# Performance work log

Measured on AMD Instinct MI355X. Metric: run time of the kernel, lower is better.

## Reference

```python
import jax, jax.numpy as jnp
import numpy as np

TOP_K = 2


def setup_inputs() -> dict:
    key = jax.random.key(0)
    ks = jax.random.split(key, 5)
    T, H, I, E = 4096, 2048, 4096, 8
    scale = 0.02
    return {
        "hidden_states": jax.random.normal(ks[0], (T, H), dtype=jnp.float32),
        "router_logits": jax.random.normal(ks[1], (T, E), dtype=jnp.float32),
        "w1": jax.random.normal(ks[2], (E, I, H), dtype=jnp.float32) * scale,
        "w3": jax.random.normal(ks[3], (E, I, H), dtype=jnp.float32) * scale,
        "w2": jax.random.normal(ks[4], (E, H, I), dtype=jnp.float32) * scale,
    }


def reference(hidden_states, router_logits, w1, w3, w2):
    # hidden_states: [T, H], router_logits: [T, E]
    E = w1.shape[0]
    # Top-k routing with softmax renormalization over the selected logits.
    topk_vals, topk_idx = jax.lax.top_k(router_logits, TOP_K)  # [T, K]
    routing_weights = jax.nn.softmax(topk_vals, axis=-1)       # [T, K]
    # combine[t, e] = sum of routing weights of slots that picked expert e
    combine = jnp.sum(
        jnp.where(topk_idx[:, :, None] == jnp.arange(E)[None, None, :],
                  routing_weights[:, :, None], 0.0),
        axis=1)  # [T, E]
    out = jnp.zeros_like(hidden_states)
    for e in range(E):  # fixed small structural loop over experts
        gate = hidden_states @ w1[e].T        # [T, I]
        up = hidden_states @ w3[e].T          # [T, I]
        y = (jax.nn.silu(gate) * up) @ w2[e].T  # [T, H]
        out = out + combine[:, e, None] * y
    return out
```

## Files before the change

kernel.cpp:

```cpp
#include <hip/hip_runtime.h>
#include <stdint.h>

#define T_TOK 4096
#define H_DIM 2048
#define I_DIM 4096
#define N_EXP 8

typedef __attribute__((ext_vector_type(8))) short bf16x8;
typedef __attribute__((ext_vector_type(4))) float f32x4;
typedef __attribute__((ext_vector_type(8))) unsigned short u16x8;

__device__ __forceinline__ unsigned short f2bf(float x) {
    union { float f; unsigned u; } v; v.f = x;
    unsigned r = v.u + 0x7FFF + ((v.u >> 16) & 1);
    return (unsigned short)(r >> 16);
}

__device__ __forceinline__ void async_cp16(const void* g, const unsigned short* lds_base) {
    __builtin_amdgcn_global_load_lds(
        (const __attribute__((address_space(1))) unsigned*)g,
        (__attribute__((address_space(3))) unsigned*)(unsigned)(uintptr_t)lds_base,
        16, 0, 0);
}

__global__ void routing_kernel(const float* __restrict__ logits,
                               int* __restrict__ counts, int* __restrict__ offsets,
                               int* __restrict__ btok, float* __restrict__ bw,
                               int* __restrict__ tok2slot) {
    __shared__ int s_cnt[N_EXP];
    __shared__ int s_off[N_EXP];
    __shared__ int s_cur[N_EXP];
    const int tid = threadIdx.x;
    if (tid < N_EXP) s_cnt[tid] = 0;
    __syncthreads();

    int e0a[16], e1a[16]; float w0a[16], w1a[16];
    #pragma unroll
    for (int it = 0; it < 16; ++it) {
        int t = tid + it * 256;
        float l[8];
        #pragma unroll
        for (int e = 0; e < 8; ++e) l[e] = logits[t * 8 + e];
        int b0 = 0; float v0 = l[0];
        #pragma unroll
        for (int e = 1; e < 8; ++e) if (l[e] > v0) { v0 = l[e]; b0 = e; }
        int b1 = (b0 == 0) ? 1 : 0; float v1 = l[b1];
        #pragma unroll
        for (int e = 0; e < 8; ++e) if (e != b0 && l[e] > v1) { v1 = l[e]; b1 = e; }
        float w0 = 1.0f / (1.0f + __expf(v1 - v0));
        e0a[it] = b0; e1a[it] = b1; w0a[it] = w0; w1a[it] = 1.0f - w0;
        atomicAdd(&s_cnt[b0], 1);
        atomicAdd(&s_cnt[b1], 1);
    }
    __syncthreads();
    if (tid == 0) {
        int acc = 0;
        for (int e = 0; e < N_EXP; ++e) { s_off[e] = acc; s_cur[e] = acc; acc += s_cnt[e]; }
    }
    __syncthreads();
    if (tid < N_EXP) { counts[tid] = s_cnt[tid]; offsets[tid] = s_off[tid]; }
    #pragma unroll
    for (int it = 0; it < 16; ++it) {
        int t = tid + it * 256;
        int p0 = atomicAdd(&s_cur[e0a[it]], 1);
        btok[p0] = t; bw[p0] = w0a[it];
        int p1 = atomicAdd(&s_cur[e1a[it]], 1);
        btok[p1] = t; bw[p1] = w1a[it];
        tok2slot[2 * t] = p0;
        tok2slot[2 * t + 1] = p1;
    }
}

__global__ void cvt_kernel(const float* __restrict__ x, unsigned short* __restrict__ xb) {
    int i = blockIdx.x * blockDim.x + threadIdx.x;
    float4 v = ((const float4*)x)[i];
    ushort4 o;
    o.x = f2bf(v.x); o.y = f2bf(v.y); o.z = f2bf(v.z); o.w = f2bf(v.w);
    ((ushort4*)xb)[i] = o;
}


__global__ __launch_bounds__(256, 2)
void gemm1f_kernel(const unsigned short* __restrict__ Xb,
                   const unsigned short* __restrict__ W1b,
                   const unsigned short* __restrict__ W3b,
                   const int* __restrict__ counts,
                   const int* __restrict__ offsets,
                   const int* __restrict__ btok,
                   unsigned short* __restrict__ hbuf) {
    const int e = blockIdx.z;
    const int ne = counts[e];
    const int mt = blockIdx.y;
    if (mt * 128 >= ne) return;
    const int nt = blockIdx.x;
    const int off = offsets[e];

    __shared__ unsigned short sA[128 * 32];
    __shared__ unsigned short sB1[128 * 32];
    __shared__ unsigned short sB3[128 * 32];
    __shared__ int s_tok[128];

    const int tid = threadIdx.x;
    if (tid < 128) {
        int slot = mt * 128 + tid;
        s_tok[tid] = btok[off + ((slot < ne) ? slot : 0)];
    }
    __syncthreads();

    const int lane = tid & 63;
    const int wv = tid >> 6;
    const int wm = (wv >> 1) << 6;
    const int wn = (wv & 1) << 6;
    const int q = lane >> 4;
    const int c = lane & 15;

    const int srow = wv * 32 + (lane >> 2);
    const int cc = (lane & 3) * 8;

    const unsigned short* gA0 = Xb + (size_t)s_tok[srow] * H_DIM + cc;
    const unsigned short* gA1 = Xb + (size_t)s_tok[srow + 16] * H_DIM + cc;
    const size_t wrow = (size_t)e * I_DIM + nt * 128 + srow;
    const unsigned short* gW1a = W1b + wrow * H_DIM + cc;
    const unsigned short* gW1b_ = W1b + (wrow + 16) * H_DIM + cc;
    const unsigned short* gW3a = W3b + wrow * H_DIM + cc;
    const unsigned short* gW3b_ = W3b + (wrow + 16) * H_DIM + cc;

    const unsigned short* dA0 = &sA[1024 * wv];
    const unsigned short* dA1 = &sA[1024 * wv + 512];
    const unsigned short* dB1a = &sB1[1024 * wv];
    const unsigned short* dB1b = &sB1[1024 * wv + 512];
    const unsigned short* dB3a = &sB3[1024 * wv];
    const unsigned short* dB3b = &sB3[1024 * wv + 512];

    f32x4 accg[4][4], accu[4][4];
    const f32x4 zero = {0.0f, 0.0f, 0.0f, 0.0f};
    #pragma unroll
    for (int i = 0; i < 4; ++i)
        #pragma unroll
        for (int j = 0; j < 4; ++j) { accg[i][j] = zero; accu[i][j] = zero; }

    for (int kt = 0; kt < H_DIM; kt += 32) {
        __syncthreads();
        async_cp16(gA0 + kt, dA0);
        async_cp16(gA1 + kt, dA1);
        async_cp16(gW1a + kt, dB1a);
        async_cp16(gW1b_ + kt, dB1b);
        async_cp16(gW3a + kt, dB3a);
        async_cp16(gW3b_ + kt, dB3b);
        __syncthreads();

        bf16x8 af[4], b1f[4], b3f[4];
        #pragma unroll
        for (int i = 0; i < 4; ++i)
            af[i] = *(const bf16x8*)(&sA[(wm + i * 16 + c) * 32 + q * 8]);
        #pragma unroll
        for (int j = 0; j < 4; ++j) {
            b1f[j] = *(const bf16x8*)(&sB1[(wn + j * 16 + c) * 32 + q * 8]);
            b3f[j] = *(const bf16x8*)(&sB3[(wn + j * 16 + c) * 32 + q * 8]);
        }
        #pragma unroll
        for (int i = 0; i < 4; ++i)
            #pragma unroll
            for (int j = 0; j < 4; ++j) {
                accg[i][j] = __builtin_amdgcn_mfma_f32_16x16x32_bf16(af[i], b1f[j], accg[i][j], 0, 0, 0);
                accu[i][j] = __builtin_amdgcn_mfma_f32_16x16x32_bf16(af[i], b3f[j], accu[i][j], 0, 0, 0);
            }
    }

    #pragma unroll
    for (int i = 0; i < 4; ++i) {
        #pragma unroll
        for (int r = 0; r < 4; ++r) {
            int mloc = wm + i * 16 + q * 4 + r;
            int slot = mt * 128 + mloc;
            if (slot < ne) {
                size_t rowbase = (size_t)(off + slot) * I_DIM + nt * 128 + wn;
                #pragma unroll
                for (int j = 0; j < 4; ++j) {
                    float g = accg[i][j][r];
                    float u = accu[i][j][r];
                    float val = (g / (1.0f + __expf(-g))) * u;
                    hbuf[rowbase + j * 16 + c] = f2bf(val);
                }
            }
        }
    }
}

__global__ __launch_bounds__(256, 2)
void gemm2f_kernel(const unsigned short* __restrict__ hbuf,
                   const unsigned short* __restrict__ W2b,
                   const int* __restrict__ counts,
                   const int* __restrict__ offsets,
                   float* __restrict__ ybuf) {
    const int e = blockIdx.z;
    const int ne = counts[e];
    const int mt = blockIdx.y;
    if (mt * 128 >= ne) return;
    const int nt = blockIdx.x;
    const int off = offsets[e];

    __shared__ unsigned short sA[128 * 32];
    __shared__ unsigned short sB[128 * 32];

    const int tid = threadIdx.x;
    const int lane = tid & 63;
    const int wv = tid >> 6;
    const int wm = (wv >> 1) << 6;
    const int wn = (wv & 1) << 6;
    const int q = lane >> 4;
    const int c = lane & 15;

    const int srow = wv * 32 + (lane >> 2);
    const int cc = (lane & 3) * 8;

    int slotA0 = mt * 128 + srow;      if (slotA0 >= ne) slotA0 = ne - 1;
    int slotA1 = mt * 128 + srow + 16; if (slotA1 >= ne) slotA1 = ne - 1;
    const unsigned short* gA0 = hbuf + (size_t)(off + slotA0) * I_DIM + cc;
    const unsigned short* gA1 = hbuf + (size_t)(off + slotA1) * I_DIM + cc;
    const size_t wrow = (size_t)e * H_DIM + nt * 128 + srow;
    const unsigned short* gB0 = W2b + wrow * I_DIM + cc;
    const unsigned short* gB1 = W2b + (wrow + 16) * I_DIM + cc;

    const unsigned short* dA0 = &sA[1024 * wv];
    const unsigned short* dA1 = &sA[1024 * wv + 512];
    const unsigned short* dB0 = &sB[1024 * wv];
    const unsigned short* dB1 = &sB[1024 * wv + 512];

    f32x4 acc[4][4];
    const f32x4 zero = {0.0f, 0.0f, 0.0f, 0.0f};
    #pragma unroll
    for (int i = 0; i < 4; ++i)
        #pragma unroll
        for (int j = 0; j < 4; ++j) acc[i][j] = zero;

    for (int kt = 0; kt < I_DIM; kt += 32) {
        __syncthreads();
        async_cp16(gA0 + kt, dA0);
        async_cp16(gA1 + kt, dA1);
        async_cp16(gB0 + kt, dB0);
        async_cp16(gB1 + kt, dB1);
        __syncthreads();

        bf16x8 af[4], bfr[4];
        #pragma unroll
        for (int i = 0; i < 4; ++i)
            af[i] = *(const bf16x8*)(&sA[(wm + i * 16 + c) * 32 + q * 8]);
        #pragma unroll
        for (int j = 0; j < 4; ++j)
            bfr[j] = *(const bf16x8*)(&sB[(wn + j * 16 + c) * 32 + q * 8]);
        #pragma unroll
        for (int i = 0; i < 4; ++i)
            #pragma unroll
            for (int j = 0; j < 4; ++j)
                acc[i][j] = __builtin_amdgcn_mfma_f32_16x16x32_bf16(af[i], bfr[j], acc[i][j], 0, 0, 0);
    }

    #pragma unroll
    for (int i = 0; i < 4; ++i) {
        #pragma unroll
        for (int r = 0; r < 4; ++r) {
            int mloc = wm + i * 16 + q * 4 + r;
            int slot = mt * 128 + mloc;
            if (slot < ne) {
                float* obase = ybuf + (size_t)(off + slot) * H_DIM + nt * 128 + wn;
                #pragma unroll
                for (int j = 0; j < 4; ++j)
                    obase[j * 16 + c] = acc[i][j][r];
            }
        }
    }
}

__global__ void combine_kernel(const float* __restrict__ ybuf,
                               const float* __restrict__ bw,
                               const int* __restrict__ tok2slot,
                               float* __restrict__ out) {
    int i = blockIdx.x * blockDim.x + threadIdx.x;
    int t = i >> 9;
    int h4 = i & 511;
    int p0 = tok2slot[2 * t], p1 = tok2slot[2 * t + 1];
    float w0 = bw[p0], w1 = bw[p1];
    float4 a = ((const float4*)(ybuf + (size_t)p0 * H_DIM))[h4];
    float4 b = ((const float4*)(ybuf + (size_t)p1 * H_DIM))[h4];
    float4 o;
    o.x = w0 * a.x + w1 * b.x;
    o.y = w0 * a.y + w1 * b.y;
    o.z = w0 * a.z + w1 * b.z;
    o.w = w0 * a.w + w1 * b.w;
    ((float4*)(out + (size_t)t * H_DIM))[h4] = o;
}


__global__ __launch_bounds__(256, 2)
void gemm1_kernel(const unsigned short* __restrict__ Xb,
                  const float* __restrict__ W1,
                  const float* __restrict__ W3,
                  const int* __restrict__ counts,
                  const int* __restrict__ offsets,
                  const int* __restrict__ btok,
                  unsigned short* __restrict__ hbuf) {
    const int e = blockIdx.z;
    const int ne = counts[e];
    const int mt = blockIdx.y;
    if (mt * 128 >= ne) return;
    const int nt = blockIdx.x;
    const int off = offsets[e];

    __shared__ unsigned short sA[128][32];
    __shared__ unsigned short sB1[128][32];
    __shared__ unsigned short sB3[128][32];
    __shared__ int s_tok[128];

    const int tid = threadIdx.x;
    if (tid < 128) {
        int slot = mt * 128 + tid;
        s_tok[tid] = (slot < ne) ? btok[off + slot] : -1;
    }

    const float* __restrict__ pB1 = W1 + (size_t)e * I_DIM * H_DIM + (size_t)(nt * 128) * H_DIM;
    const float* __restrict__ pB3 = W3 + (size_t)e * I_DIM * H_DIM + (size_t)(nt * 128) * H_DIM;

    const int lane = tid & 63;
    const int wv = tid >> 6;
    const int wm = (wv >> 1) << 6;
    const int wn = (wv & 1) << 6;
    const int q = lane >> 4;
    const int c = lane & 15;

    f32x4 accg[4][4], accu[4][4];
    const f32x4 zero = {0.0f, 0.0f, 0.0f, 0.0f};
    #pragma unroll
    for (int i = 0; i < 4; ++i)
        #pragma unroll
        for (int j = 0; j < 4; ++j) { accg[i][j] = zero; accu[i][j] = zero; }

    const int srow = tid >> 2;
    const int schunk = (tid & 3) * 8;

    for (int kt = 0; kt < H_DIM; kt += 32) {
        __syncthreads();
        #pragma unroll
        for (int p = 0; p < 2; ++p) {
            int r = srow + p * 64;
            int tok = s_tok[r];
            u16x8 av = {0, 0, 0, 0, 0, 0, 0, 0};
            if (tok >= 0)
                av = *(const u16x8*)(Xb + (size_t)tok * H_DIM + kt + schunk);
            *(u16x8*)(&sA[r][schunk]) = av;

            const float* b1 = pB1 + (size_t)r * H_DIM + kt + schunk;
            float4 x0 = *(const float4*)(b1);
            float4 x1 = *(const float4*)(b1 + 4);
            u16x8 bv;
            bv[0] = f2bf(x0.x); bv[1] = f2bf(x0.y); bv[2] = f2bf(x0.z); bv[3] = f2bf(x0.w);
            bv[4] = f2bf(x1.x); bv[5] = f2bf(x1.y); bv[6] = f2bf(x1.z); bv[7] = f2bf(x1.w);
            *(u16x8*)(&sB1[r][schunk]) = bv;

            const float* b3 = pB3 + (size_t)r * H_DIM + kt + schunk;
            float4 y0 = *(const float4*)(b3);
            float4 y1 = *(const float4*)(b3 + 4);
            u16x8 cv;
            cv[0] = f2bf(y0.x); cv[1] = f2bf(y0.y); cv[2] = f2bf(y0.z); cv[3] = f2bf(y0.w);
            cv[4] = f2bf(y1.x); cv[5] = f2bf(y1.y); cv[6] = f2bf(y1.z); cv[7] = f2bf(y1.w);
            *(u16x8*)(&sB3[r][schunk]) = cv;
        }
        __syncthreads();

        bf16x8 af[4], b1f[4], b3f[4];
        #pragma unroll
        for (int i = 0; i < 4; ++i)
            af[i] = *(const bf16x8*)(&sA[wm + i * 16 + c][q * 8]);
        #pragma unroll
        for (int j = 0; j < 4; ++j) {
            b1f[j] = *(const bf16x8*)(&sB1[wn + j * 16 + c][q * 8]);
            b3f[j] = *(const bf16x8*)(&sB3[wn + j * 16 + c][q * 8]);
        }
        #pragma unroll
        for (int i = 0; i < 4; ++i)
            #pragma unroll
            for (int j = 0; j < 4; ++j) {
                accg[i][j] = __builtin_amdgcn_mfma_f32_16x16x32_bf16(af[i], b1f[j], accg[i][j], 0, 0, 0);
                accu[i][j] = __builtin_amdgcn_mfma_f32_16x16x32_bf16(af[i], b3f[j], accu[i][j], 0, 0, 0);
            }
    }

    #pragma unroll
    for (int i = 0; i < 4; ++i) {
        #pragma unroll
        for (int r = 0; r < 4; ++r) {
            int mloc = wm + i * 16 + q * 4 + r;
            int slot = mt * 128 + mloc;
            if (slot < ne) {
                size_t rowbase = (size_t)(off + slot) * I_DIM + nt * 128 + wn;
                #pragma unroll
                for (int j = 0; j < 4; ++j) {
                    float g = accg[i][j][r];
                    float u = accu[i][j][r];
                    float val = (g / (1.0f + __expf(-g))) * u;
                    hbuf[rowbase + j * 16 + c] = f2bf(val);
                }
            }
        }
    }
}

__global__ __launch_bounds__(256, 2)
void gemm2_kernel(const unsigned short* __restrict__ hbuf,
                  const float* __restrict__ W2,
                  const int* __restrict__ counts,
                  const int* __restrict__ offsets,
                  const int* __restrict__ btok,
                  const float* __restrict__ bw,
                  float* __restrict__ out) {
    const int e = blockIdx.z;
    const int ne = counts[e];
    const int mt = blockIdx.y;
    if (mt * 128 >= ne) return;
    const int nt = blockIdx.x;
    const int off = offsets[e];

    __shared__ unsigned short sA[128][32];
    __shared__ unsigned short sB[128][32];

    const int tid = threadIdx.x;
    const int lane = tid & 63;
    const int wv = tid >> 6;
    const int wm = (wv >> 1) << 6;
    const int wn = (wv & 1) << 6;
    const int q = lane >> 4;
    const int c = lane & 15;

    const float* __restrict__ pB = W2 + (size_t)e * H_DIM * I_DIM + (size_t)(nt * 128) * I_DIM;

    f32x4 acc[4][4];
    const f32x4 zero = {0.0f, 0.0f, 0.0f, 0.0f};
    #pragma unroll
    for (int i = 0; i < 4; ++i)
        #pragma unroll
        for (int j = 0; j < 4; ++j) acc[i][j] = zero;

    const int srow = tid >> 2;
    const int schunk = (tid & 3) * 8;

    for (int kt = 0; kt < I_DIM; kt += 32) {
        __syncthreads();
        #pragma unroll
        for (int p = 0; p < 2; ++p) {
            int r = srow + p * 64;
            int slot = mt * 128 + r;
            u16x8 av = {0, 0, 0, 0, 0, 0, 0, 0};
            if (slot < ne)
                av = *(const u16x8*)(hbuf + (size_t)(off + slot) * I_DIM + kt + schunk);
            *(u16x8*)(&sA[r][schunk]) = av;

            const float* b = pB + (size_t)r * I_DIM + kt + schunk;
            float4 x0 = *(const float4*)(b);
            float4 x1 = *(const float4*)(b + 4);
            u16x8 bv;
            bv[0] = f2bf(x0.x); bv[1] = f2bf(x0.y); bv[2] = f2bf(x0.z); bv[3] = f2bf(x0.w);
            bv[4] = f2bf(x1.x); bv[5] = f2bf(x1.y); bv[6] = f2bf(x1.z); bv[7] = f2bf(x1.w);
            *(u16x8*)(&sB[r][schunk]) = bv;
        }
        __syncthreads();

        bf16x8 af[4], bfr[4];
        #pragma unroll
        for (int i = 0; i < 4; ++i)
            af[i] = *(const bf16x8*)(&sA[wm + i * 16 + c][q * 8]);
        #pragma unroll
        for (int j = 0; j < 4; ++j)
            bfr[j] = *(const bf16x8*)(&sB[wn + j * 16 + c][q * 8]);
        #pragma unroll
        for (int i = 0; i < 4; ++i)
            #pragma unroll
            for (int j = 0; j < 4; ++j)
                acc[i][j] = __builtin_amdgcn_mfma_f32_16x16x32_bf16(af[i], bfr[j], acc[i][j], 0, 0, 0);
    }

    #pragma unroll
    for (int i = 0; i < 4; ++i) {
        #pragma unroll
        for (int r = 0; r < 4; ++r) {
            int mloc = wm + i * 16 + q * 4 + r;
            int slot = mt * 128 + mloc;
            if (slot < ne) {
                int tok = btok[off + slot];
                float wgt = bw[off + slot];
                float* obase = out + (size_t)tok * H_DIM + nt * 128 + wn;
                #pragma unroll
                for (int j = 0; j < 4; ++j)
                    atomicAdd(obase + j * 16 + c, wgt * acc[i][j][r]);
            }
        }
    }
}


extern "C" void kernel_launch(void* const* d_in, const int* in_sizes, int n_in,
                              void* d_out, int out_size, void* d_ws, size_t ws_size,
                              hipStream_t stream) {
    const float* hs = (const float*)d_in[0];
    const float* rl = (const float*)d_in[1];
    const float* w1 = (const float*)d_in[2];
    const float* w3 = (const float*)d_in[3];
    const float* w2 = (const float*)d_in[4];
    float* out = (float*)d_out;

    char* ws = (char*)d_ws;
    int*   counts   = (int*)(ws);
    int*   offsets  = (int*)(ws + 256);
    int*   btok     = (int*)(ws + 4096);
    float* bw       = (float*)(ws + 36864);
    int*   tok2slot = (int*)(ws + 69632);

    const size_t MB = 1ull << 20;
    const size_t NEED_A = 529 * MB;

    if (ws_size >= NEED_A) {
        unsigned short* Xb   = (unsigned short*)(ws + 1 * MB);
        unsigned short* hbuf = (unsigned short*)(ws + 17 * MB);
        float*          ybuf = (float*)(ws + 81 * MB);
        unsigned short* w1b  = (unsigned short*)(ws + 145 * MB);
        unsigned short* w3b  = (unsigned short*)(ws + 273 * MB);
        unsigned short* w2b  = (unsigned short*)(ws + 401 * MB);

        routing_kernel<<<1, 256, 0, stream>>>(rl, counts, offsets, btok, bw, tok2slot);

        cvt_kernel<<<(T_TOK * H_DIM / 4) / 256, 256, 0, stream>>>(hs, Xb);
        int wn4 = N_EXP * I_DIM * H_DIM / 4;
        cvt_kernel<<<wn4 / 256, 256, 0, stream>>>(w1, w1b);
        cvt_kernel<<<wn4 / 256, 256, 0, stream>>>(w3, w3b);
        cvt_kernel<<<wn4 / 256, 256, 0, stream>>>(w2, w2b);

        gemm1f_kernel<<<dim3(I_DIM / 128, 64, N_EXP), 256, 0, stream>>>(
            Xb, w1b, w3b, counts, offsets, btok, hbuf);

        gemm2f_kernel<<<dim3(H_DIM / 128, 64, N_EXP), 256, 0, stream>>>(
            hbuf, w2b, counts, offsets, ybuf);

        combine_kernel<<<(T_TOK * (H_DIM / 4)) / 256, 256, 0, stream>>>(
            ybuf, bw, tok2slot, out);
    } else {
        unsigned short* Xb   = (unsigned short*)(ws + 1 * MB);
        unsigned short* hbuf = (unsigned short*)(ws + 32 * MB);

        hipMemsetAsync(out, 0, (size_t)T_TOK * H_DIM * sizeof(float), stream);

        routing_kernel<<<1, 256, 0, stream>>>(rl, counts, offsets, btok, bw, tok2slot);

        cvt_kernel<<<(T_TOK * H_DIM / 4) / 256, 256, 0, stream>>>(hs, Xb);

        gemm1_kernel<<<dim3(I_DIM / 128, T_TOK / 128, N_EXP), 256, 0, stream>>>(
            Xb, w1, w3, counts, offsets, btok, hbuf);

        gemm2_kernel<<<dim3(H_DIM / 128, T_TOK / 128, N_EXP), 256, 0, stream>>>(
            hbuf, w2, counts, offsets, btok, bw, out);
    }
}
```

Baseline: 1.369 ms.

## Triple-buffer MoE GEMMs with larger 256-row tiles, LDS swizzle, and interleaved prefetch

```diff
diff --git a/kernel.cpp b/kernel.cpp
--- a/kernel.cpp
+++ b/kernel.cpp
@@ -80,8 +80,8 @@
 }
 
 
-__global__ __launch_bounds__(256, 2)
-void gemm1f_kernel(const unsigned short* __restrict__ Xb,
+__global__ __launch_bounds__(512, 2)
+void gemm1p_kernel(const unsigned short* __restrict__ Xb,
                    const unsigned short* __restrict__ W1b,
                    const unsigned short* __restrict__ W3b,
                    const int* __restrict__ counts,
@@ -91,19 +91,19 @@
     const int e = blockIdx.z;
     const int ne = counts[e];
     const int mt = blockIdx.y;
-    if (mt * 128 >= ne) return;
+    if (mt * 256 >= ne) return;
     const int nt = blockIdx.x;
     const int off = offsets[e];
 
-    __shared__ unsigned short sA[128 * 32];
-    __shared__ unsigned short sB1[128 * 32];
-    __shared__ unsigned short sB3[128 * 32];
-    __shared__ int s_tok[128];
+    __shared__ unsigned short sA[3][256 * 32];
+    __shared__ unsigned short sB1[3][128 * 32];
+    __shared__ unsigned short sB3[3][128 * 32];
+    __shared__ int s_tok[256];
 
     const int tid = threadIdx.x;
-    if (tid < 128) {
-        int slot = mt * 128 + tid;
-        s_tok[tid] = btok[off + ((slot < ne) ? slot : 0)];
+    if (tid < 256) {
+        int slot = mt * 256 + tid;
+        s_tok[tid] = btok[off + ((slot < ne) ? slot : (ne - 1))];
     }
     __syncthreads();
 
@@ -113,24 +113,23 @@
     const int wn = (wv & 1) << 6;
     const int q = lane >> 4;
     const int c = lane & 15;
-
-    const int srow = wv * 32 + (lane >> 2);
-    const int cc = (lane & 3) * 8;
-
-    const unsigned short* gA0 = Xb + (size_t)s_tok[srow] * H_DIM + cc;
-    const unsigned short* gA1 = Xb + (size_t)s_tok[srow + 16] * H_DIM + cc;
+    const int xq = q ^ ((c >> 1) & 3);
+
+    const int aoff = (wm + c) * 32 + xq * 8;
+    const int boff = (wn + c) * 32 + xq * 8;
+
+    const int srow = wv * 16 + (lane >> 2);
+    const int sg = (lane & 3) ^ ((lane >> 3) & 3);
+
+    const unsigned short* gA0 = Xb + (size_t)s_tok[srow] * H_DIM + sg * 8;
+    const unsigned short* gA1 = Xb + (size_t)s_tok[srow + 128] * H_DIM + sg * 8;
     const size_t wrow = (size_t)e * I_DIM + nt * 128 + srow;
-    const unsigned short* gW1a = W1b + wrow * H_DIM + cc;
-    const unsigned short* gW1b_ = W1b + (wrow + 16) * H_DIM + cc;
-    const unsigned short* gW3a = W3b + wrow * H_DIM + cc;
-    const unsigned short* gW3b_ = W3b + (wrow + 16) * H_DIM + cc;
-
-    const unsigned short* dA0 = &sA[1024 * wv];
-    const unsigned short* dA1 = &sA[1024 * wv + 512];
-    const unsigned short* dB1a = &sB1[1024 * wv];
-    const unsigned short* dB1b = &sB1[1024 * wv + 512];
-    const unsigned short* dB3a = &sB3[1024 * wv];
-    const unsigned short* dB3b = &sB3[1024 * wv + 512];
+    const unsigned short* gB1 = W1b + wrow * H_DIM + sg * 8;
+    const unsigned short* gB3 = W3b + wrow * H_DIM + sg * 8;
+
+    const int dofsA0 = wv * 512;
+    const int dofsA1 = 4096 + wv * 512;
+    const int dofsB  = wv * 512;
 
     f32x4 accg[4][4], accu[4][4];
     const f32x4 zero = {0.0f, 0.0f, 0.0f, 0.0f};
@@ -139,32 +138,66 @@
         #pragma unroll
         for (int j = 0; j < 4; ++j) { accg[i][j] = zero; accu[i][j] = zero; }
 
-    for (int kt = 0; kt < H_DIM; kt += 32) {
-        __syncthreads();
-        async_cp16(gA0 + kt, dA0);
-        async_cp16(gA1 + kt, dA1);
-        async_cp16(gW1a + kt, dB1a);
-        async_cp16(gW1b_ + kt, dB1b);
-        async_cp16(gW3a + kt, dB3a);
-        async_cp16(gW3b_ + kt, dB3b);
-        __syncthreads();
-
-        bf16x8 af[4], b1f[4], b3f[4];
-        #pragma unroll
-        for (int i = 0; i < 4; ++i)
-            af[i] = *(const bf16x8*)(&sA[(wm + i * 16 + c) * 32 + q * 8]);
-        #pragma unroll
-        for (int j = 0; j < 4; ++j) {
-            b1f[j] = *(const bf16x8*)(&sB1[(wn + j * 16 + c) * 32 + q * 8]);
-            b3f[j] = *(const bf16x8*)(&sB3[(wn + j * 16 + c) * 32 + q * 8]);
-        }
+    async_cp16(gA0,      &sA[0][dofsA0]);
+    async_cp16(gB1,      &sB1[0][dofsB]);
+    async_cp16(gA1,      &sA[0][dofsA1]);
+    async_cp16(gB3,      &sB3[0][dofsB]);
+    async_cp16(gA0 + 32, &sA[1][dofsA0]);
+    async_cp16(gB1 + 32, &sB1[1][dofsB]);
+    async_cp16(gA1 + 32, &sA[1][dofsA1]);
+    async_cp16(gB3 + 32, &sB3[1][dofsB]);
+    asm volatile("s_waitcnt vmcnt(4)" ::: "memory");
+    __builtin_amdgcn_s_barrier();
+    __builtin_amdgcn_sched_barrier(0);
+
+    const int NT = H_DIM / 32;
+    for (int t = 0; t < NT; ++t) {
+        const int cur = t % 3;
+        const int nx2 = (t + 2) % 3;
+        const bool stg = (t + 2) < NT;
+        const int kt2 = (t + 2) * 32;
+
+        bf16x8 af[4], b1f[4];
+        #pragma unroll
+        for (int i = 0; i < 4; ++i) af[i] = *(const bf16x8*)(&sA[cur][aoff + i * 512]);
+        #pragma unroll
+        for (int j = 0; j < 4; ++j) b1f[j] = *(const bf16x8*)(&sB1[cur][boff + j * 512]);
+        if (stg) {
+            async_cp16(gA0 + kt2, &sA[nx2][dofsA0]);
+            async_cp16(gB1 + kt2, &sB1[nx2][dofsB]);
+        }
+        __builtin_amdgcn_s_barrier();
+        __builtin_amdgcn_s_setprio(1);
         #pragma unroll
         for (int i = 0; i < 4; ++i)
             #pragma unroll
-            for (int j = 0; j < 4; ++j) {
+            for (int j = 0; j < 4; ++j)
                 accg[i][j] = __builtin_amdgcn_mfma_f32_16x16x32_bf16(af[i], b1f[j], accg[i][j], 0, 0, 0);
+        __builtin_amdgcn_s_setprio(0);
+        __builtin_amdgcn_s_barrier();
+
+        bf16x8 b3f[4];
+        #pragma unroll
+        for (int j = 0; j < 4; ++j) b3f[j] = *(const bf16x8*)(&sB3[cur][boff + j * 512]);
+        if (stg) {
+            async_cp16(gA1 + kt2, &sA[nx2][dofsA1]);
+            async_cp16(gB3 + kt2, &sB3[nx2][dofsB]);
+        }
+        __builtin_amdgcn_s_barrier();
+        __builtin_amdgcn_s_setprio(1);
+        #pragma unroll
+        for (int i = 0; i < 4; ++i)
+            #pragma unroll
+            for (int j = 0; j < 4; ++j)
                 accu[i][j] = __builtin_amdgcn_mfma_f32_16x16x32_bf16(af[i], b3f[j], accu[i][j], 0, 0, 0);
-            }
+        __builtin_amdgcn_s_setprio(0);
+
+        if (t + 1 < NT) {
+            if (stg) asm volatile("s_waitcnt vmcnt(4)" ::: "memory");
+            else     asm volatile("s_waitcnt vmcnt(0)" ::: "memory");
+            __builtin_amdgcn_s_barrier();
+            __builtin_amdgcn_sched_barrier(0);
+        }
     }
 
     #pragma unroll
@@ -172,7 +205,7 @@
         #pragma unroll
         for (int r = 0; r < 4; ++r) {
             int mloc = wm + i * 16 + q * 4 + r;
-            int slot = mt * 128 + mloc;
+            int slot = mt * 256 + mloc;
             if (slot < ne) {
                 size_t rowbase = (size_t)(off + slot) * I_DIM + nt * 128 + wn;
                 #pragma unroll
@@ -187,8 +220,8 @@
     }
 }
 
-__global__ __launch_bounds__(256, 2)
-void gemm2f_kernel(const unsigned short* __restrict__ hbuf,
+__global__ __launch_bounds__(512, 2)
+void gemm2p_kernel(const unsigned short* __restrict__ hbuf,
                    const unsigned short* __restrict__ W2b,
                    const int* __restrict__ counts,
                    const int* __restrict__ offsets,
@@ -196,74 +229,116 @@
     const int e = blockIdx.z;
     const int ne = counts[e];
     const int mt = blockIdx.y;
-    if (mt * 128 >= ne) return;
+    if (mt * 256 >= ne) return;
     const int nt = blockIdx.x;
     const int off = offsets[e];
 
-    __shared__ unsigned short sA[128 * 32];
-    __shared__ unsigned short sB[128 * 32];
+    __shared__ unsigned short sA[3][256 * 32];
+    __shared__ unsigned short sB[3][256 * 32];
 
     const int tid = threadIdx.x;
     const int lane = tid & 63;
     const int wv = tid >> 6;
-    const int wm = (wv >> 1) << 6;
-    const int wn = (wv & 1) << 6;
+    const int wm = (wv >> 2) << 7;
+    const int wn = (wv & 3) << 6;
     const int q = lane >> 4;
     const int c = lane & 15;
-
-    const int srow = wv * 32 + (lane >> 2);
-    const int cc = (lane & 3) * 8;
-
-    int slotA0 = mt * 128 + srow;      if (slotA0 >= ne) slotA0 = ne - 1;
-    int slotA1 = mt * 128 + srow + 16; if (slotA1 >= ne) slotA1 = ne - 1;
-    const unsigned short* gA0 = hbuf + (size_t)(off + slotA0) * I_DIM + cc;
-    const unsigned short* gA1 = hbuf + (size_t)(off + slotA1) * I_DIM + cc;
-    const size_t wrow = (size_t)e * H_DIM + nt * 128 + srow;
-    const unsigned short* gB0 = W2b + wrow * I_DIM + cc;
-    const unsigned short* gB1 = W2b + (wrow + 16) * I_DIM + cc;
-
-    const unsigned short* dA0 = &sA[1024 * wv];
-    const unsigned short* dA1 = &sA[1024 * wv + 512];
-    const unsigned short* dB0 = &sB[1024 * wv];
-    const unsigned short* dB1 = &sB[1024 * wv + 512];
-
-    f32x4 acc[4][4];
+    const int xq = q ^ ((c >> 1) & 3);
+
+    const int aoff = (wm + c) * 32 + xq * 8;
+    const int boff = (wn + c) * 32 + xq * 8;
+
+    const int srow = wv * 16 + (lane >> 2);
+    const int sg = (lane & 3) ^ ((lane >> 3) & 3);
+
+    int slot0 = mt * 256 + srow;        if (slot0 >= ne) slot0 = ne - 1;
+    int slot1 = mt * 256 + srow + 128;  if (slot1 >= ne) slot1 = ne - 1;
+    const unsigned short* gA0 = hbuf + (size_t)(off + slot0) * I_DIM + sg * 8;
+    const unsigned short* gA1 = hbuf + (size_t)(off + slot1) * I_DIM + sg * 8;
+    const size_t wrow = (size_t)e * H_DIM + nt * 256 + srow;
+    const unsigned short* gB0 = W2b + wrow * I_DIM + sg * 8;
+    const unsigned short* gB1 = W2b + (wrow + 128) * I_DIM + sg * 8;
+
+    const int dofs0 = wv * 512;
+    const int dofs1 = 4096 + wv * 512;
+
+    f32x4 acc[8][4];
     const f32x4 zero = {0.0f, 0.0f, 0.0f, 0.0f};
     #pragma unroll
-    for (int i = 0; i < 4; ++i)
+    for (int i = 0; i < 8; ++i)
         #pragma unroll
         for (int j = 0; j < 4; ++j) acc[i][j] = zero;
 
-    for (int kt = 0; kt < I_DIM; kt += 32) {
-        __syncthreads();
-        async_cp16(gA0 + kt, dA0);
-        async_cp16(gA1 + kt, dA1);
-        async_cp16(gB0 + kt, dB0);
-        async_cp16(gB1 + kt, dB1);
-        __syncthreads();
+    async_cp16(gA0,      &sA[0][dofs0]);
+    async_cp16(gB0,      &sB[0][dofs0]);
+    async_cp16(gA1,      &sA[0][dofs1]);
+    async_cp16(gB1,      &sB[0][dofs1]);
+    async_cp16(gA0 + 32, &sA[1][dofs0]);
+    async_cp16(gB0 + 32, &sB[1][dofs0]);
+    async_cp16(gA1 + 32, &sA[1][dofs1]);
+    async_cp16(gB1 + 32, &sB[1][dofs1]);
+    asm volatile("s_waitcnt vmcnt(4)" ::: "memory");
+    __builtin_amdgcn_s_barrier();
+    __builtin_amdgcn_sched_barrier(0);
+
+    const int NT = I_DIM / 32;
+    for (int t = 0; t < NT; ++t) {
+        const int cur = t % 3;
+        const int nx2 = (t + 2) % 3;
+        const bool stg = (t + 2) < NT;
+        const int kt2 = (t + 2) * 32;
 
         bf16x8 af[4], bfr[4];
         #pragma unroll
-        for (int i = 0; i < 4; ++i)
-            af[i] = *(const bf16x8*)(&sA[(wm + i * 16 + c) * 32 + q * 8]);
-        #pragma unroll
-        for (int j = 0; j < 4; ++j)
-            bfr[j] = *(const bf16x8*)(&sB[(wn + j * 16 + c) * 32 + q * 8]);
+        for (int i = 0; i < 4; ++i) af[i] = *(const bf16x8*)(&sA[cur][aoff + i * 512]);
+        #pragma unroll
+        for (int j = 0; j < 4; ++j) bfr[j] = *(const bf16x8*)(&sB[cur][boff + j * 512]);
+        if (stg) {
+            async_cp16(gA0 + kt2, &sA[nx2][dofs0]);
+            async_cp16(gB0 + kt2, &sB[nx2][dofs0]);
+        }
+        __builtin_amdgcn_s_barrier();
+        __builtin_amdgcn_s_setprio(1);
         #pragma unroll
         for (int i = 0; i < 4; ++i)
             #pragma unroll
             for (int j = 0; j < 4; ++j)
                 acc[i][j] = __builtin_amdgcn_mfma_f32_16x16x32_bf16(af[i], bfr[j], acc[i][j], 0, 0, 0);
-    }
-
-    #pragma unroll
-    for (int i = 0; i < 4; ++i) {
+        __builtin_amdgcn_s_setprio(0);
+        __builtin_amdgcn_s_barrier();
+
+        bf16x8 af2[4];
+        #pragma unroll
+        for (int i = 0; i < 4; ++i) af2[i] = *(const bf16x8*)(&sA[cur][aoff + (i + 4) * 512]);
+        if (stg) {
+            async_cp16(gA1 + kt2, &sA[nx2][dofs1]);
+            async_cp16(gB1 + kt2, &sB[nx2][dofs1]);
+        }
+        __builtin_amdgcn_s_barrier();
+        __builtin_amdgcn_s_setprio(1);
+        #pragma unroll
+        for (int i = 0; i < 4; ++i)
+            #pragma unroll
+            for (int j = 0; j < 4; ++j)
+                acc[i + 4][j] = __builtin_amdgcn_mfma_f32_16x16x32_bf16(af2[i], bfr[j], acc[i + 4][j], 0, 0, 0);
+        __builtin_amdgcn_s_setprio(0);
+
+        if (t + 1 < NT) {
+            if (stg) asm volatile("s_waitcnt vmcnt(4)" ::: "memory");
+            else     asm volatile("s_waitcnt vmcnt(0)" ::: "memory");
+            __builtin_amdgcn_s_barrier();
+            __builtin_amdgcn_sched_barrier(0);
+        }
+    }
+
+    #pragma unroll
+    for (int i = 0; i < 8; ++i) {
         #pragma unroll
         for (int r = 0; r < 4; ++r) {
             int mloc = wm + i * 16 + q * 4 + r;
-            int slot = mt * 128 + mloc;
+            int slot = mt * 256 + mloc;
             if (slot < ne) {
-                float* obase = ybuf + (size_t)(off + slot) * H_DIM + nt * 128 + wn;
+                float* obase = ybuf + (size_t)(off + slot) * H_DIM + nt * 256 + wn;
                 #pragma unroll
                 for (int j = 0; j < 4; ++j)
                     obase[j * 16 + c] = acc[i][j][r];
@@ -533,10 +608,10 @@
         cvt_kernel<<<wn4 / 256, 256, 0, stream>>>(w3, w3b);
         cvt_kernel<<<wn4 / 256, 256, 0, stream>>>(w2, w2b);
 
-        gemm1f_kernel<<<dim3(I_DIM / 128, 64, N_EXP), 256, 0, stream>>>(
+        gemm1p_kernel<<<dim3(I_DIM / 128, 32, N_EXP), 512, 0, stream>>>(
             Xb, w1b, w3b, counts, offsets, btok, hbuf);
 
-        gemm2f_kernel<<<dim3(H_DIM / 128, 64, N_EXP), 256, 0, stream>>>(
+        gemm2p_kernel<<<dim3(H_DIM / 256, 32, N_EXP), 512, 0, stream>>>(
             hbuf, w2b, counts, offsets, ybuf);
 
         combine_kernel<<<(T_TOK * (H_DIM / 4)) / 256, 256, 0, stream>>>(
```

Result: faster. 1.276 ms (-6.8%).
